# Optimization experiments

Measured on AMD Instinct MI355X. Metric: run time of the kernel, lower is better.

The kernel has to match this reference:

```python
import jax, jax.numpy as jnp
import numpy as np


def softmax_kernel(data, projection, is_query, eps=1e-4):
    # data: [b,h,n,d], projection: [m,d]
    d = data.shape[-1]
    data_normalizer = d ** -0.25
    ratio = projection.shape[0] ** -0.5
    data_dash = jnp.einsum('bhnd,md->bhnm', data_normalizer * data, projection)
    diag_data = (data ** 2).sum(axis=-1) * 0.5 * (data_normalizer ** 2)  # [b,h,n]
    diag_data = diag_data[..., None]
    if is_query:
        m = jnp.max(data_dash, axis=-1, keepdims=True)  # per-query max
    else:
        m = jnp.max(data_dash)  # global max over all keys
    return ratio * (jnp.exp(data_dash - diag_data - m) + eps)


def linear_attention(q, k, v):
    # q,k: [b,h,n,m] feature maps; v: [b,h,n,e]
    D_inv = 1.0 / jnp.einsum('bhnm,bhm->bhn', q, k.sum(axis=-2))
    context = jnp.einsum('bhnm,bhne->bhme', k, v)
    return jnp.einsum('bhme,bhnm,bhn->bhne', context, q, D_inv)


def setup_inputs() -> dict:
    key = jax.random.key(0)
    k1, k2, k3, k4 = jax.random.split(key, 4)
    B, H, N, D, M = 4, 16, 4096, 64, 256
    # gaussian orthogonal random matrix (scaling=0): 4 orthogonal DxD blocks,
    # rows rescaled by norms of gaussian rows
    blocks = []
    kk = k4
    for _ in range(M // D):
        kk, sub = jax.random.split(kk)
        g = jax.random.normal(sub, (D, D), dtype=jnp.float32)
        qmat, _ = jnp.linalg.qr(g)
        blocks.append(qmat.T)
    final = jnp.concatenate(blocks, axis=0)  # [M, D]
    kk, sub = jax.random.split(kk)
    multiplier = jnp.linalg.norm(jax.random.normal(sub, (M, D), dtype=jnp.float32), axis=1)
    proj = multiplier[:, None] * final
    return {
        'q': jax.random.normal(k1, (B, H, N, D), dtype=jnp.float32),
        'k': jax.random.normal(k2, (B, H, N, D), dtype=jnp.float32),
        'v': jax.random.normal(k3, (B, H, N, D), dtype=jnp.float32),
        'projection': proj,
    }


def reference(q, k, v, projection):
    q_prime = softmax_kernel(q, projection, is_query=True)
    k_prime = softmax_kernel(k, projection, is_query=False)
    return linear_attention(q_prime, k_prime, v)
```

## Files before the change

### kernel.cpp

```cpp
#include <hip/hip_runtime.h>
#include <hip/hip_bf16.h>


#define BH    64
#define NSEQ  4096
#define DD    64
#define MM    256
#define DN    0.35355339059327373f
#define RATIO 0.0625f
#define EPS   1e-4f
#define NSEG  8

#define CTX_OFF  0
#define KSUM_OFF (BH*MM*DD)
#define VSUM_OFF (KSUM_OFF + BH*MM)
#define MG_OFF   (VSUM_OFF + BH*DD)
#define CTX_SLICE (BH*MM*DD)

typedef __attribute__((ext_vector_type(8)))  short bf16x8;
typedef __attribute__((ext_vector_type(16))) float f32x16;

#define MFMA(a,b,c) __builtin_amdgcn_mfma_f32_32x32x16_bf16((a),(b),(c),0,0,0)
#define PATROW(r,h) ((((r)&3) + 8*((r)>>2)) + 4*(h))

__device__ __forceinline__ unsigned short f2bf(float x) {
    unsigned u = __float_as_uint(x);
    return (unsigned short)((u + 0x7fffu + ((u >> 16) & 1u)) >> 16);
}
__device__ __forceinline__ bf16x8 hi8(const float* x) {
    union { short s[8]; bf16x8 v; } r;
#pragma unroll
    for (int i = 0; i < 8; ++i) r.s[i] = (short)f2bf(x[i]);
    return r.v;
}
__device__ __forceinline__ unsigned ford(float f) {
    unsigned u = __float_as_uint(f);
    return (u & 0x80000000u) ? ~u : (u | 0x80000000u);
}
__device__ __forceinline__ float ford_inv(unsigned u) {
    return (u & 0x80000000u) ? __uint_as_float(u & 0x7fffffffu) : __uint_as_float(~u);
}
__device__ __forceinline__ unsigned pkbf(float lo, float hi) {
    union { __hip_bfloat162 b2; unsigned u; } cvt;
    cvt.b2 = __float22bfloat162_rn(make_float2(lo, hi));
    return cvt.u;
}
template<int BASE>
__device__ __forceinline__ bf16x8 repack8(const f32x16& a, int h) {
    unsigned X0 = pkbf(a[BASE+0], a[BASE+1]);
    unsigned X1 = pkbf(a[BASE+2], a[BASE+3]);
    unsigned Y0 = pkbf(a[BASE+4], a[BASE+5]);
    unsigned Y1 = pkbf(a[BASE+6], a[BASE+7]);
    unsigned tX0 = (unsigned)__shfl_xor((int)X0, 32);
    unsigned tX1 = (unsigned)__shfl_xor((int)X1, 32);
    unsigned tY0 = (unsigned)__shfl_xor((int)Y0, 32);
    unsigned tY1 = (unsigned)__shfl_xor((int)Y1, 32);
    union { unsigned w[4]; bf16x8 v; } r;
    r.w[0] = h ? tY0 : X0;
    r.w[1] = h ? tY1 : X1;
    r.w[2] = h ? Y0 : tX0;
    r.w[3] = h ? Y1 : tX1;
    return r.v;
}
#define VSWZ(e) ((((e)&7) ^ ((e)>>3)) << 3)

__global__ __launch_bounds__(512, 2)
void keys_kernel(const float* __restrict__ kg, const float* __restrict__ vg,
                 const float* __restrict__ pg, float* __restrict__ ws,
                 float* __restrict__ outp)
{
    __shared__ __align__(16) short kf[2][8*1024];
    __shared__ __align__(16) short vT[2][64*128];
    __shared__ float diagl[2][128];
    __shared__ float vswr[8][64];

    const int tid  = threadIdx.x;
    const int wv   = tid >> 6;
    const int lane = tid & 63;
    const int l31  = lane & 31;
    const int h    = lane >> 5;
    const int bh   = blockIdx.x >> 3;
    const int seg  = blockIdx.x & 7;

    bf16x8 pBh[4];
    {
        const int m = 32*wv + l31;
#pragma unroll
        for (int ks = 0; ks < 4; ++ks) {
            const int d0 = 16*ks + 8*h;
            float x[8];
            *(float4*)&x[0] = *(const float4*)(pg + m*64 + d0);
            *(float4*)&x[4] = *(const float4*)(pg + m*64 + d0 + 4);
            pBh[ks] = hi8(x);
        }
    }

    f32x16 cacc0, cacc1;
#pragma unroll
    for (int i = 0; i < 16; ++i) { cacc0[i] = 0.f; cacc1[i] = 0.f; }
    float ksacc = 0.f, mloc = -3e38f;
    float vsacc[16];
#pragma unroll
    for (int i = 0; i < 16; ++i) vsacc[i] = 0.f;

    auto stage = [&](int ch, int b) {
        const int n = tid >> 2, q = tid & 3;
        const size_t base = ((size_t)(bh*NSEQ + seg*512 + ch*128 + n)) * 64 + q*16;
        float x[16], y[16];
        *(float4*)&x[0]  = *(const float4*)(kg + base);
        *(float4*)&x[4]  = *(const float4*)(kg + base + 4);
        *(float4*)&x[8]  = *(const float4*)(kg + base + 8);
        *(float4*)&x[12] = *(const float4*)(kg + base + 12);
        *(float4*)&y[0]  = *(const float4*)(vg + base);
        *(float4*)&y[4]  = *(const float4*)(vg + base + 4);
        *(float4*)&y[8]  = *(const float4*)(vg + base + 8);
        *(float4*)&y[12] = *(const float4*)(vg + base + 12);
        float ss = 0.f;
#pragma unroll
        for (int i = 0; i < 16; ++i) { x[i] *= DN; ss += x[i]*x[i]; }
        ss += __shfl_xor(ss, 1); ss += __shfl_xor(ss, 2);
        if (q == 0) diagl[b][n] = 0.5f * ss;
        const int dg0 = 2*q, dg1 = 2*q + 1;
        *(bf16x8*)&kf[b][dg0*1024 + ((n*8) ^ (dg0*8))] = hi8(x);
        *(bf16x8*)&kf[b][dg1*1024 + ((n*8) ^ (dg1*8))] = hi8(x + 8);
#pragma unroll
        for (int i = 0; i < 16; ++i) {
            vsacc[i] += y[i];
            const int e = q*16 + i;
            vT[b][e*128 + (n ^ VSWZ(e))] = (short)f2bf(y[i]);
        }
    };

    auto sgemm = [&](int b, int hf, f32x16& r0, f32x16& r1) {
#pragma unroll
        for (int i = 0; i < 16; ++i) { r0[i] = 0.f; r1[i] = 0.f; }
#pragma unroll
        for (int ks = 0; ks < 4; ++ks) {
            const int dg = ks*2 + h;
            const int ofs = dg*1024 + ((((64*hf) + l31)*8) ^ (dg*8));
            bf16x8 a0 = *(const bf16x8*)&kf[b][ofs];
            bf16x8 a1 = *(const bf16x8*)&kf[b][ofs + 256];
            r0 = MFMA(a0, pBh[ks], r0);
            r1 = MFMA(a1, pBh[ks], r1);
        }
    };

    auto expack = [&](int b, int hf, f32x16& t0, f32x16& t1, bf16x8* wfr) {
        float kp = 0.f;
#pragma unroll
        for (int g = 0; g < 4; ++g) {
            const float4 dq0 = *(const float4*)&diagl[b][64*hf + 8*g + 4*h];
            const float4 dq1 = *(const float4*)&diagl[b][64*hf + 32 + 8*g + 4*h];
            const float d0[4] = {dq0.x, dq0.y, dq0.z, dq0.w};
            const float d1[4] = {dq1.x, dq1.y, dq1.z, dq1.w};
#pragma unroll
            for (int j = 0; j < 4; ++j) {
                const int r = 4*g + j;
                mloc = fmaxf(mloc, t0[r]);
                const float w0 = __expf(t0[r] - d0[j]);
                t0[r] = w0; kp += w0;
                mloc = fmaxf(mloc, t1[r]);
                const float w1 = __expf(t1[r] - d1[j]);
                t1[r] = w1; kp += w1;
            }
        }
        ksacc += kp;
        wfr[0] = repack8<0>(t0, h);
        wfr[1] = repack8<8>(t0, h);
        wfr[2] = repack8<0>(t1, h);
        wfr[3] = repack8<8>(t1, h);
    };

    auto ctxg = [&](int b, int hf, const bf16x8* wfr) {
#pragma unroll
        for (int ks = 0; ks < 4; ++ks) {
            const int nb = 64*hf + 16*ks + 8*h;
            const int e0 = l31, e1 = l31 + 32;
            bf16x8 b0 = *(const bf16x8*)&vT[b][e0*128 + (nb ^ VSWZ(e0))];
            bf16x8 b1 = *(const bf16x8*)&vT[b][e1*128 + (nb ^ VSWZ(e1))];
            cacc0 = MFMA(wfr[ks], b0, cacc0);
            cacc1 = MFMA(wfr[ks], b1, cacc1);
        }
    };

    stage(0, 0);
    __syncthreads();
    f32x16 sA0, sA1;
    sgemm(0, 0, sA0, sA1);

    for (int ch = 0; ch < 4; ++ch) {
        const int bc = ch & 1, bn = bc ^ 1;
        if (ch < 3) stage(ch + 1, bn);

        bf16x8 wfrA[4];
        expack(bc, 0, sA0, sA1, wfrA);
        f32x16 sB0, sB1;
        __builtin_amdgcn_s_setprio(1);
        sgemm(bc, 1, sB0, sB1);
        ctxg(bc, 0, wfrA);
        __builtin_amdgcn_s_setprio(0);
        bf16x8 wfrB[4];
        expack(bc, 1, sB0, sB1, wfrB);
        ctxg(bc, 1, wfrB);
        __syncthreads();
        if (ch < 3) {
            __builtin_amdgcn_s_setprio(1);
            sgemm(bn, 0, sA0, sA1);
            __builtin_amdgcn_s_setprio(0);
        }
    }

    ksacc += __shfl_xor(ksacc, 32);
    if (h == 0) atomicAdd(&ws[KSUM_OFF + bh*MM + 32*wv + l31], ksacc);

#pragma unroll
    for (int m = 1; m <= 32; m <<= 1) mloc = fmaxf(mloc, __shfl_xor(mloc, m));
    if (lane == 0) atomicMax((unsigned*)&ws[MG_OFF], ford(mloc));

    {
        float* cb = outp + (size_t)(seg*BH + bh) * (MM*DD);
#pragma unroll
        for (int r = 0; r < 16; ++r) {
            const int m = 32*wv + PATROW(r, h);
            cb[m*64 + l31]      = cacc0[r];
            cb[m*64 + l31 + 32] = cacc1[r];
        }
    }

#pragma unroll
    for (int i = 0; i < 16; ++i) {
        float v = vsacc[i];
        v += __shfl_xor(v, 4); v += __shfl_xor(v, 8);
        v += __shfl_xor(v, 16); v += __shfl_xor(v, 32);
        vsacc[i] = v;
    }
    if (lane < 4) {
#pragma unroll
        for (int i = 0; i < 16; ++i) vswr[wv][lane*16 + i] = vsacc[i];
    }
    __syncthreads();
    if (tid < 64) {
        float s = 0.f;
#pragma unroll
        for (int w = 0; w < 8; ++w) s += vswr[w][tid];
        atomicAdd(&ws[VSUM_OFF + bh*DD + tid], s);
    }
}

__global__ __launch_bounds__(512)
void reduce_kernel(const float* __restrict__ outp, float* __restrict__ ws)
{
    const int idx = blockIdx.x * 512 + threadIdx.x;
    const float4* o4 = (const float4*)outp;
    float4 s = o4[idx];
#pragma unroll
    for (int sl = 1; sl < NSEG; ++sl) {
        float4 t = o4[sl*(CTX_SLICE/4) + idx];
        s.x += t.x; s.y += t.y; s.z += t.z; s.w += t.w;
    }
    ((float4*)(ws + CTX_OFF))[idx] = s;
}

__global__ __launch_bounds__(512, 2)
void query_kernel(const float* __restrict__ qg, const float* __restrict__ pg,
                  const float* __restrict__ ws, float* __restrict__ out)
{
    __shared__ __align__(16) short pfh[MM*DD];
    __shared__ __align__(16) short ctxb[32*64*8];
    __shared__ float ksuml[MM];
    __shared__ float ctxsuml[DD];
    __shared__ float ksumsuml;
    __shared__ float epsl[8][32];
    __shared__ float denl[8][32];

    const int tid  = threadIdx.x;
    const int wv   = tid >> 6;
    const int lane = tid & 63;
    const int l31  = lane & 31;
    const int h    = lane >> 5;
    const int bh   = blockIdx.x >> 3;
    const int seg  = blockIdx.x & 7;

    const float mg = ford_inv(*(const unsigned*)&ws[MG_OFF]);
    const float cs = RATIO * __expf(-mg);
    const float ce = RATIO * EPS;

    if (tid < DD) ctxsuml[tid] = 0.f;
    if (tid == 0) ksumsuml = 0.f;
    __syncthreads();

    {
        const int m = tid >> 1, dh = tid & 1;
#pragma unroll
        for (int b = 0; b < 4; ++b) {
            const int d0 = dh*32 + b*8;
            float x[8];
            *(float4*)&x[0] = *(const float4*)(pg + m*64 + d0);
            *(float4*)&x[4] = *(const float4*)(pg + m*64 + d0 + 4);
            const int g = ((m>>5)*4 + (d0>>4))*2 + ((d0>>3)&1);
            *(bf16x8*)&pfh[(g*32 + (m&31))*8] = hi8(x);
        }
    }
#pragma unroll
    for (int it = 0; it < 4; ++it) {
        const int gid = it*512 + tid;
        const int g = gid >> 6, e = gid & 63;
        const int mb = (g>>1)*16 + (g&1)*8;
        const float vs = ws[VSUM_OFF + bh*DD + e];
        float part = 0.f;
        union { short s[8]; bf16x8 v; } tmp;
#pragma unroll
        for (int j = 0; j < 8; ++j) {
            const float x = cs*ws[CTX_OFF + (size_t)bh*(MM*DD) + (mb+j)*64 + e] + ce*vs;
            part += x;
            tmp.s[j] = (short)f2bf(x);
        }
        *(bf16x8*)&ctxb[(g*64 + e)*8] = tmp.v;
        atomicAdd(&ctxsuml[e], part);
    }
    if (tid < 256) {
        const float kt = cs*ws[KSUM_OFF + bh*MM + tid] + ce*(float)NSEQ;
        ksuml[tid] = kt;
        atomicAdd(&ksumsuml, kt);
    }
    __syncthreads();

    const float cs0 = ctxsuml[l31];
    const float cs1 = ctxsuml[l31 + 32];
    const float kss = ksumsuml;

    for (int ch = 0; ch < 2; ++ch) {
        const int rown = seg*512 + ch*256 + wv*32;
        const size_t gn = (size_t)(bh*NSEQ + rown + l31);

        bf16x8 qbh[4];
        float ss = 0.f;
#pragma unroll
        for (int ks = 0; ks < 4; ++ks) {
            const int d0 = 16*ks + 8*h;
            float x[8];
            *(float4*)&x[0] = *(const float4*)(qg + gn*64 + d0);
            *(float4*)&x[4] = *(const float4*)(qg + gn*64 + d0 + 4);
#pragma unroll
            for (int i = 0; i < 8; ++i) { x[i] *= DN; ss += x[i]*x[i]; }
            qbh[ks] = hi8(x);
        }
        const float diag = 0.5f * (ss + __shfl_xor(ss, 32));

        f32x16 n0, n1;
#pragma unroll
        for (int i = 0; i < 16; ++i) { n0[i] = 0.f; n1[i] = 0.f; }
        float den = 0.f, mx = -3e38f;
#pragma unroll
        for (int mt = 0; mt < 8; ++mt) {
            f32x16 s;
#pragma unroll
            for (int i = 0; i < 16; ++i) s[i] = 0.f;
#pragma unroll
            for (int ks = 0; ks < 4; ++ks) {
                const int g = (mt*4 + ks)*2 + h;
                bf16x8 ah = *(const bf16x8*)&pfh[(g*32 + l31)*8];
                s = MFMA(ah, qbh[ks], s);
            }
#pragma unroll
            for (int r = 0; r < 16; ++r) mx = fmaxf(mx, s[r]);
#pragma unroll
            for (int r = 0; r < 16; ++r) {
                const float u = __expf(s[r] - diag);
                s[r] = u;
                den = fmaf(u, ksuml[mt*32 + PATROW(r, h)], den);
            }
            bf16x8 t0 = repack8<0>(s, h);
            bf16x8 t1 = repack8<8>(s, h);
            const int g0 = 4*mt + h, g1 = 4*mt + 2 + h;
            n0 = MFMA(t0, *(const bf16x8*)&ctxb[(g0*64 + l31)*8],      n0);
            n1 = MFMA(t0, *(const bf16x8*)&ctxb[(g0*64 + l31 + 32)*8], n1);
            n0 = MFMA(t1, *(const bf16x8*)&ctxb[(g1*64 + l31)*8],      n0);
            n1 = MFMA(t1, *(const bf16x8*)&ctxb[(g1*64 + l31 + 32)*8], n1);
        }

        mx  = fmaxf(mx, __shfl_xor(mx, 32));
        den += __shfl_xor(den, 32);
        const float epsp = EPS * __expf(mx);
        const float denf = den + epsp * kss;
        if (h == 0) { epsl[wv][l31] = epsp; denl[wv][l31] = denf; }
        asm volatile("s_waitcnt lgkmcnt(0)" ::: "memory");

#pragma unroll
        for (int r = 0; r < 16; ++r) {
            const int nn = PATROW(r, h);
            const float e1  = epsl[wv][nn];
            const float rdn = 1.0f / denl[wv][nn];
            float* op = out + ((size_t)(bh*NSEQ + rown + nn))*64;
            op[l31]      = (n0[r] + e1*cs0) * rdn;
            op[l31 + 32] = (n1[r] + e1*cs1) * rdn;
        }
    }
}

extern "C" void kernel_launch(void* const* d_in, const int* in_sizes, int n_in,
                              void* d_out, int out_size, void* d_ws, size_t ws_size,
                              hipStream_t stream)
{
    const float* q = (const float*)d_in[0];
    const float* k = (const float*)d_in[1];
    const float* v = (const float*)d_in[2];
    const float* p = (const float*)d_in[3];
    float* ws  = (float*)d_ws;
    float* out = (float*)d_out;

    (void)hipMemsetAsync((void*)(ws + KSUM_OFF),
                         0, (size_t)(BH*MM + BH*DD + 4) * sizeof(float), stream);
    keys_kernel<<<dim3(512), dim3(512), 0, stream>>>(k, v, p, ws, out);
    reduce_kernel<<<dim3(512), dim3(512), 0, stream>>>(out, ws);
    query_kernel<<<dim3(512), dim3(512), 0, stream>>>(q, p, ws, out);
}
```

Measured before the change: 167.6 us.

## Restructure key kernel into 64-row chunks with register-prefetched loads and packed bf16 conversion

The keys kernel now handles 64-row chunks over 8 iterations instead of 128-row chunks over 4. Global loads of the next chunk go into registers before the compute, and the shared-memory writes happen after the context MFMAs, which halves LDS buffer size. V is loaded transposed per thread so each thread packs one bf16x8 vector instead of 16 scalar shorts, and the v-sum reduction collapses to a single value per lane. The DN scaling is folded into the projection instead of each key/query row, and bf16 conversion uses the packed hardware intrinsic. The changes risk uncoalesced strided V loads and more loop iterations with syncthreads.

```diff
diff --git a/kernel.cpp b/kernel.cpp
--- a/kernel.cpp
+++ b/kernel.cpp
@@ -23,27 +23,29 @@
 #define MFMA(a,b,c) __builtin_amdgcn_mfma_f32_32x32x16_bf16((a),(b),(c),0,0,0)
 #define PATROW(r,h) ((((r)&3) + 8*((r)>>2)) + 4*(h))
 
-__device__ __forceinline__ unsigned short f2bf(float x) {
-    unsigned u = __float_as_uint(x);
-    return (unsigned short)((u + 0x7fffu + ((u >> 16) & 1u)) >> 16);
-}
-__device__ __forceinline__ bf16x8 hi8(const float* x) {
-    union { short s[8]; bf16x8 v; } r;
-#pragma unroll
-    for (int i = 0; i < 8; ++i) r.s[i] = (short)f2bf(x[i]);
-    return r.v;
-}
-__device__ __forceinline__ unsigned ford(float f) {
-    unsigned u = __float_as_uint(f);
-    return (u & 0x80000000u) ? ~u : (u | 0x80000000u);
-}
-__device__ __forceinline__ float ford_inv(unsigned u) {
-    return (u & 0x80000000u) ? __uint_as_float(u & 0x7fffffffu) : __uint_as_float(~u);
-}
 __device__ __forceinline__ unsigned pkbf(float lo, float hi) {
     union { __hip_bfloat162 b2; unsigned u; } cvt;
     cvt.b2 = __float22bfloat162_rn(make_float2(lo, hi));
     return cvt.u;
+}
+__device__ __forceinline__ bf16x8 hi8(const float* x) {
+    union { unsigned w[4]; bf16x8 v; } r;
+    r.w[0] = pkbf(x[0], x[1]);
+    r.w[1] = pkbf(x[2], x[3]);
+    r.w[2] = pkbf(x[4], x[5]);
+    r.w[3] = pkbf(x[6], x[7]);
+    return r.v;
+}
+__device__ __forceinline__ unsigned short f2bf(float x) {
+    unsigned u = __float_as_uint(x);
+    return (unsigned short)((u + 0x7fffu + ((u >> 16) & 1u)) >> 16);
+}
+__device__ __forceinline__ unsigned ford(float f) {
+    unsigned u = __float_as_uint(f);
+    return (u & 0x80000000u) ? ~u : (u | 0x80000000u);
+}
+__device__ __forceinline__ float ford_inv(unsigned u) {
+    return (u & 0x80000000u) ? __uint_as_float(u & 0x7fffffffu) : __uint_as_float(~u);
 }
 template<int BASE>
 __device__ __forceinline__ bf16x8 repack8(const f32x16& a, int h) {
@@ -62,16 +64,15 @@
     r.w[3] = h ? Y1 : tX1;
     return r.v;
 }
-#define VSWZ(e) ((((e)&7) ^ ((e)>>3)) << 3)
 
 __global__ __launch_bounds__(512, 2)
 void keys_kernel(const float* __restrict__ kg, const float* __restrict__ vg,
                  const float* __restrict__ pg, float* __restrict__ ws,
                  float* __restrict__ outp)
 {
-    __shared__ __align__(16) short kf[2][8*1024];
-    __shared__ __align__(16) short vT[2][64*128];
-    __shared__ float diagl[2][128];
+    __shared__ __align__(16) short kf[2][64*64];
+    __shared__ __align__(16) short vT[2][64*64];
+    __shared__ float diagl[2][64];
     __shared__ float vswr[8][64];
 
     const int tid  = threadIdx.x;
@@ -82,6 +83,9 @@
     const int bh   = blockIdx.x >> 3;
     const int seg  = blockIdx.x & 7;
 
+    const int kn = tid >> 3, kdg = tid & 7;
+    const int ve = tid & 63, vnr = tid >> 6;
+
     bf16x8 pBh[4];
     {
         const int m = 32*wv + l31;
@@ -91,6 +95,8 @@
             float x[8];
             *(float4*)&x[0] = *(const float4*)(pg + m*64 + d0);
             *(float4*)&x[4] = *(const float4*)(pg + m*64 + d0 + 4);
+#pragma unroll
+            for (int i = 0; i < 8; ++i) x[i] *= DN;
             pBh[ks] = hi8(x);
         }
     }
@@ -98,46 +104,38 @@
     f32x16 cacc0, cacc1;
 #pragma unroll
     for (int i = 0; i < 16; ++i) { cacc0[i] = 0.f; cacc1[i] = 0.f; }
-    float ksacc = 0.f, mloc = -3e38f;
-    float vsacc[16];
-#pragma unroll
-    for (int i = 0; i < 16; ++i) vsacc[i] = 0.f;
-
-    auto stage = [&](int ch, int b) {
-        const int n = tid >> 2, q = tid & 3;
-        const size_t base = ((size_t)(bh*NSEQ + seg*512 + ch*128 + n)) * 64 + q*16;
-        float x[16], y[16];
-        *(float4*)&x[0]  = *(const float4*)(kg + base);
-        *(float4*)&x[4]  = *(const float4*)(kg + base + 4);
-        *(float4*)&x[8]  = *(const float4*)(kg + base + 8);
-        *(float4*)&x[12] = *(const float4*)(kg + base + 12);
-        *(float4*)&y[0]  = *(const float4*)(vg + base);
-        *(float4*)&y[4]  = *(const float4*)(vg + base + 4);
-        *(float4*)&y[8]  = *(const float4*)(vg + base + 8);
-        *(float4*)&y[12] = *(const float4*)(vg + base + 12);
+    float ksacc = 0.f, mloc = -3e38f, vsacc = 0.f;
+
+    float kx[8], vx[8];
+
+    auto loads = [&](int ch) {
+        const size_t kb = ((size_t)(bh*NSEQ + seg*512 + ch*64 + kn)) * 64 + kdg*8;
+        *(float4*)&kx[0] = *(const float4*)(kg + kb);
+        *(float4*)&kx[4] = *(const float4*)(kg + kb + 4);
+        const size_t vb = ((size_t)(bh*NSEQ + seg*512 + ch*64 + vnr*8)) * 64 + ve;
+#pragma unroll
+        for (int j = 0; j < 8; ++j) vx[j] = vg[vb + (size_t)j*64];
+    };
+
+    auto stage_write = [&](int b) {
         float ss = 0.f;
 #pragma unroll
-        for (int i = 0; i < 16; ++i) { x[i] *= DN; ss += x[i]*x[i]; }
-        ss += __shfl_xor(ss, 1); ss += __shfl_xor(ss, 2);
-        if (q == 0) diagl[b][n] = 0.5f * ss;
-        const int dg0 = 2*q, dg1 = 2*q + 1;
-        *(bf16x8*)&kf[b][dg0*1024 + ((n*8) ^ (dg0*8))] = hi8(x);
-        *(bf16x8*)&kf[b][dg1*1024 + ((n*8) ^ (dg1*8))] = hi8(x + 8);
-#pragma unroll
-        for (int i = 0; i < 16; ++i) {
-            vsacc[i] += y[i];
-            const int e = q*16 + i;
-            vT[b][e*128 + (n ^ VSWZ(e))] = (short)f2bf(y[i]);
-        }
+        for (int i = 0; i < 8; ++i) ss = fmaf(kx[i], kx[i], ss);
+        ss += __shfl_xor(ss, 1); ss += __shfl_xor(ss, 2); ss += __shfl_xor(ss, 4);
+        if (kdg == 0) diagl[b][kn] = ss * 0.0625f;
+        *(bf16x8*)&kf[b][kdg*512 + ((kn*8) ^ (kdg*8))] = hi8(kx);
+#pragma unroll
+        for (int j = 0; j < 8; ++j) vsacc += vx[j];
+        *(bf16x8*)&vT[b][ve*64 + ((vnr*8) ^ (8*(ve & 7)))] = hi8(vx);
     };
 
-    auto sgemm = [&](int b, int hf, f32x16& r0, f32x16& r1) {
+    auto sgemm = [&](int b, f32x16& r0, f32x16& r1) {
 #pragma unroll
         for (int i = 0; i < 16; ++i) { r0[i] = 0.f; r1[i] = 0.f; }
 #pragma unroll
         for (int ks = 0; ks < 4; ++ks) {
             const int dg = ks*2 + h;
-            const int ofs = dg*1024 + ((((64*hf) + l31)*8) ^ (dg*8));
+            const int ofs = dg*512 + ((l31*8) ^ (dg*8));
             bf16x8 a0 = *(const bf16x8*)&kf[b][ofs];
             bf16x8 a1 = *(const bf16x8*)&kf[b][ofs + 256];
             r0 = MFMA(a0, pBh[ks], r0);
@@ -145,69 +143,60 @@
         }
     };
 
-    auto expack = [&](int b, int hf, f32x16& t0, f32x16& t1, bf16x8* wfr) {
-        float kp = 0.f;
-#pragma unroll
-        for (int g = 0; g < 4; ++g) {
-            const float4 dq0 = *(const float4*)&diagl[b][64*hf + 8*g + 4*h];
-            const float4 dq1 = *(const float4*)&diagl[b][64*hf + 32 + 8*g + 4*h];
-            const float d0[4] = {dq0.x, dq0.y, dq0.z, dq0.w};
-            const float d1[4] = {dq1.x, dq1.y, dq1.z, dq1.w};
-#pragma unroll
-            for (int j = 0; j < 4; ++j) {
-                const int r = 4*g + j;
-                mloc = fmaxf(mloc, t0[r]);
-                const float w0 = __expf(t0[r] - d0[j]);
-                t0[r] = w0; kp += w0;
-                mloc = fmaxf(mloc, t1[r]);
-                const float w1 = __expf(t1[r] - d1[j]);
-                t1[r] = w1; kp += w1;
+    loads(0);
+    stage_write(0);
+    __syncthreads();
+
+    for (int ch = 0; ch < 8; ++ch) {
+        const int bc = ch & 1, bn = bc ^ 1;
+        if (ch < 7) loads(ch + 1);
+
+        f32x16 s0, s1;
+        __builtin_amdgcn_s_setprio(1);
+        sgemm(bc, s0, s1);
+        __builtin_amdgcn_s_setprio(0);
+
+        {
+            float kp = 0.f;
+#pragma unroll
+            for (int g = 0; g < 4; ++g) {
+                const float4 dq0 = *(const float4*)&diagl[bc][8*g + 4*h];
+                const float4 dq1 = *(const float4*)&diagl[bc][32 + 8*g + 4*h];
+                const float d0[4] = {dq0.x, dq0.y, dq0.z, dq0.w};
+                const float d1[4] = {dq1.x, dq1.y, dq1.z, dq1.w};
+#pragma unroll
+                for (int j = 0; j < 4; ++j) {
+                    const int r = 4*g + j;
+                    mloc = fmaxf(mloc, s0[r]);
+                    const float w0 = __expf(s0[r] - d0[j]);
+                    s0[r] = w0; kp += w0;
+                    mloc = fmaxf(mloc, s1[r]);
+                    const float w1 = __expf(s1[r] - d1[j]);
+                    s1[r] = w1; kp += w1;
+                }
             }
-        }
-        ksacc += kp;
-        wfr[0] = repack8<0>(t0, h);
-        wfr[1] = repack8<8>(t0, h);
-        wfr[2] = repack8<0>(t1, h);
-        wfr[3] = repack8<8>(t1, h);
-    };
-
-    auto ctxg = [&](int b, int hf, const bf16x8* wfr) {
+            ksacc += kp;
+        }
+        bf16x8 wfr[4];
+        wfr[0] = repack8<0>(s0, h);
+        wfr[1] = repack8<8>(s0, h);
+        wfr[2] = repack8<0>(s1, h);
+        wfr[3] = repack8<8>(s1, h);
+
+        __builtin_amdgcn_s_setprio(1);
 #pragma unroll
         for (int ks = 0; ks < 4; ++ks) {
-            const int nb = 64*hf + 16*ks + 8*h;
-            const int e0 = l31, e1 = l31 + 32;
-            bf16x8 b0 = *(const bf16x8*)&vT[b][e0*128 + (nb ^ VSWZ(e0))];
-            bf16x8 b1 = *(const bf16x8*)&vT[b][e1*128 + (nb ^ VSWZ(e1))];
+            const int nb = 16*ks + 8*h;
+            const int sw = 8*(l31 & 7);
+            bf16x8 b0 = *(const bf16x8*)&vT[bc][l31*64      + (nb ^ sw)];
+            bf16x8 b1 = *(const bf16x8*)&vT[bc][(l31+32)*64 + (nb ^ sw)];
             cacc0 = MFMA(wfr[ks], b0, cacc0);
             cacc1 = MFMA(wfr[ks], b1, cacc1);
         }
-    };
-
-    stage(0, 0);
-    __syncthreads();
-    f32x16 sA0, sA1;
-    sgemm(0, 0, sA0, sA1);
-
-    for (int ch = 0; ch < 4; ++ch) {
-        const int bc = ch & 1, bn = bc ^ 1;
-        if (ch < 3) stage(ch + 1, bn);
-
-        bf16x8 wfrA[4];
-        expack(bc, 0, sA0, sA1, wfrA);
-        f32x16 sB0, sB1;
-        __builtin_amdgcn_s_setprio(1);
-        sgemm(bc, 1, sB0, sB1);
-        ctxg(bc, 0, wfrA);
         __builtin_amdgcn_s_setprio(0);
-        bf16x8 wfrB[4];
-        expack(bc, 1, sB0, sB1, wfrB);
-        ctxg(bc, 1, wfrB);
+
+        if (ch < 7) stage_write(bn);
         __syncthreads();
-        if (ch < 3) {
-            __builtin_amdgcn_s_setprio(1);
-            sgemm(bn, 0, sA0, sA1);
-            __builtin_amdgcn_s_setprio(0);
-        }
     }
 
     ksacc += __shfl_xor(ksacc, 32);
@@ -227,17 +216,7 @@
         }
     }
 
-#pragma unroll
-    for (int i = 0; i < 16; ++i) {
-        float v = vsacc[i];
-        v += __shfl_xor(v, 4); v += __shfl_xor(v, 8);
-        v += __shfl_xor(v, 16); v += __shfl_xor(v, 32);
-        vsacc[i] = v;
-    }
-    if (lane < 4) {
-#pragma unroll
-        for (int i = 0; i < 16; ++i) vswr[wv][lane*16 + i] = vsacc[i];
-    }
+    vswr[wv][lane] = vsacc;
     __syncthreads();
     if (tid < 64) {
         float s = 0.f;
@@ -297,6 +276,8 @@
             float x[8];
             *(float4*)&x[0] = *(const float4*)(pg + m*64 + d0);
             *(float4*)&x[4] = *(const float4*)(pg + m*64 + d0 + 4);
+#pragma unroll
+            for (int i = 0; i < 8; ++i) x[i] *= DN;
             const int g = ((m>>5)*4 + (d0>>4))*2 + ((d0>>3)&1);
             *(bf16x8*)&pfh[(g*32 + (m&31))*8] = hi8(x);
         }
@@ -308,14 +289,13 @@
         const int mb = (g>>1)*16 + (g&1)*8;
         const float vs = ws[VSUM_OFF + bh*DD + e];
         float part = 0.f;
-        union { short s[8]; bf16x8 v; } tmp;
+        float xv[8];
 #pragma unroll
         for (int j = 0; j < 8; ++j) {
-            const float x = cs*ws[CTX_OFF + (size_t)bh*(MM*DD) + (mb+j)*64 + e] + ce*vs;
-            part += x;
-            tmp.s[j] = (short)f2bf(x);
-        }
-        *(bf16x8*)&ctxb[(g*64 + e)*8] = tmp.v;
+            xv[j] = cs*ws[CTX_OFF + (size_t)bh*(MM*DD) + (mb+j)*64 + e] + ce*vs;
+            part += xv[j];
+        }
+        *(bf16x8*)&ctxb[(g*64 + e)*8] = hi8(xv);
         atomicAdd(&ctxsuml[e], part);
     }
     if (tid < 256) {
@@ -342,10 +322,10 @@
             *(float4*)&x[0] = *(const float4*)(qg + gn*64 + d0);
             *(float4*)&x[4] = *(const float4*)(qg + gn*64 + d0 + 4);
 #pragma unroll
-            for (int i = 0; i < 8; ++i) { x[i] *= DN; ss += x[i]*x[i]; }
+            for (int i = 0; i < 8; ++i) ss = fmaf(x[i], x[i], ss);
             qbh[ks] = hi8(x);
         }
-        const float diag = 0.5f * (ss + __shfl_xor(ss, 32));
+        const float diag = (ss + __shfl_xor(ss, 32)) * 0.0625f;
 
         f32x16 n0, n1;
 #pragma unroll
```

Measured after the change: 141.6 us. 15.5% less time.
